# Kernel tuning notes

Hardware: AMD Instinct MI355X
Metric: run time of the kernel (lower is better)

## Reference

```python
import jax, jax.numpy as jnp
import numpy as np

N, E, IN_DIM, H, D = 50000, 1600000, 128, 4, 32
LEAKY_ALPHA = 0.2

def _glorot(key, shape):
    r = np.sqrt(6.0 / (shape[0] + shape[1]))
    return jax.random.uniform(key, shape, jnp.float32, -r, r)

def setup_inputs() -> dict:
    key = jax.random.key(0)
    ks = jax.random.split(key, 6)
    x = jax.random.normal(ks[0], (N, IN_DIM), jnp.float32)
    edge_index = jax.random.randint(ks[1], (2, E), 0, N, jnp.int64 if jax.config.jax_enable_x64 else jnp.int32)
    W_src = _glorot(ks[2], (IN_DIM, H * D))
    W_dst = _glorot(ks[3], (IN_DIM, H * D))
    W_val = _glorot(ks[4], (IN_DIM, H * D))
    attn_vec = _glorot(ks[5], (1, H)).reshape(1, H, 1) * jnp.ones((1, H, D), jnp.float32)
    # faithful glorot for (1,H,D): fan based on shape[0]+shape[1]=1+H as in source
    r = np.sqrt(6.0 / (1 + H))
    attn_vec = jax.random.uniform(jax.random.fold_in(key, 7), (1, H, D), jnp.float32, -r, r)
    return {"x": x, "edge_index": edge_index, "W_src": W_src, "W_dst": W_dst, "W_val": W_val, "attn_vec": attn_vec}

def reference(x, edge_index, W_src, W_dst, W_val, attn_vec):
    n = x.shape[0]
    h = attn_vec.shape[1]
    d = attn_vec.shape[2]
    h_s = (x @ W_src).reshape(n, h, d)
    h_d = (x @ W_dst).reshape(n, h, d)
    h_v = (x @ W_val).reshape(n, h, d)
    src, dst = edge_index[0], edge_index[1]
    # GATv2 edge scores: a^T LeakyReLU(W_src h_i + W_dst h_j)  -> [E, H]
    middle = jax.nn.leaky_relu(h_s[src] + h_d[dst], negative_slope=LEAKY_ALPHA)
    scores = jnp.sum(middle * attn_vec, axis=-1)  # [E, H]
    # segment softmax over incoming edges of each dst node (all heads at once)
    seg_max = jax.ops.segment_max(scores, dst, num_segments=n)  # [N, H]
    exp_scores = jnp.exp(scores - seg_max[dst])
    seg_sum = jax.ops.segment_sum(exp_scores, dst, num_segments=n)
    attn = exp_scores / (seg_sum[dst] + 1e-9)  # [E, H]
    # weighted message aggregation
    messages = (attn[..., None] * h_v[src]).reshape(-1, h * d)  # [E, H*D]
    out_sum = jax.ops.segment_sum(messages, dst, num_segments=n)  # [N, H*D]
    return out_sum, attn
```

## Files before the change

kernel.cpp:

```cpp
#include <hip/hip_runtime.h>

#define LEAKY 0.2f
#define BCAP 512

typedef __attribute__((ext_vector_type(8))) short short8v;
typedef __attribute__((ext_vector_type(4))) float f32x4;

__device__ __forceinline__ float h2f(unsigned short b) {
    union { unsigned short u; _Float16 h; } c; c.u = b; return (float)c.h;
}
__device__ __forceinline__ unsigned short f2h(float f) {
    union { unsigned short u; _Float16 h; } c; c.h = (_Float16)f; return c.u;
}
__device__ __forceinline__ void h4w(unsigned wx, unsigned wy, float& a, float& b, float& c, float& d) {
    a = h2f((unsigned short)(wx & 0xFFFF)); b = h2f((unsigned short)(wx >> 16));
    c = h2f((unsigned short)(wy & 0xFFFF)); d = h2f((unsigned short)(wy >> 16));
}
__device__ __forceinline__ unsigned short f2bf(float f) {
    unsigned u = __float_as_uint(f);
    return (unsigned short)((u + 0x7FFFu + ((u >> 16) & 1u)) >> 16);
}
__device__ __forceinline__ float bf2f(unsigned short b) {
    return __uint_as_float((unsigned)b << 16);
}
__device__ __forceinline__ int clampi(int v, int hi) { return v < 0 ? 0 : (v > hi ? hi : v); }
__device__ __forceinline__ int ld_idx(const int* __restrict__ ei, int is64, size_t pos) {
    return is64 ? ei[pos * 2] : ei[pos];
}

__global__ __launch_bounds__(256) void detect_kernel(const int* __restrict__ ei, int* flag) {
    __shared__ int nz;
    if (threadIdx.x == 0) nz = 0;
    __syncthreads();
    if (ei[2 * threadIdx.x + 1] != 0) atomicOr(&nz, 1);
    __syncthreads();
    if (threadIdx.x == 0) *flag = (nz == 0) ? 1 : 0;
}

__global__ __launch_bounds__(256) void zerob_kernel(int* __restrict__ bcnt, int NB8) {
    int t = blockIdx.x * 256 + threadIdx.x;
    if (t < NB8) bcnt[t] = 0;
}

__global__ __launch_bounds__(256) void bucket_scatter_kernel(
    const int* __restrict__ ei, const int* __restrict__ iflag,
    int* __restrict__ bcnt, uint2* __restrict__ bucket_data, int N, int E)
{
    int t = blockIdx.x * 256 + threadIdx.x;
    if (t >= E) return;
    int is64 = *iflag;
    int src = clampi(ld_idx(ei, is64, (size_t)t), N - 1);
    int dst = clampi(ld_idx(ei, is64, (size_t)E + t), N - 1);
    int slot = (dst >> 6) * 8 + (blockIdx.x & 7);
    int k = atomicAdd(&bcnt[slot], 1);
    if (k < BCAP)
        bucket_data[(size_t)slot * BCAP + k] =
            make_uint2((unsigned)src | ((unsigned)(dst & 63) << 16), (unsigned)t);
}

__global__ __launch_bounds__(256) void bscan_kernel(
    const int* __restrict__ bcnt, int* __restrict__ bbase,
    int* __restrict__ offs, int NB, int N, int E)
{
    __shared__ int buf[256];
    __shared__ int base;
    const int t = threadIdx.x;
    if (t == 0) { base = 0; bbase[0] = 0; offs[N] = E; }
    __syncthreads();
    for (int start = 0; start < NB; start += 256) {
        int i = start + t;
        int v = 0;
        if (i < NB) {
            #pragma unroll
            for (int s = 0; s < 8; ++s) {
                int c = bcnt[i * 8 + s];
                v += (c < BCAP ? c : BCAP);
            }
        }
        buf[t] = v;
        __syncthreads();
        #pragma unroll
        for (int off = 1; off < 256; off <<= 1) {
            int xv = (t >= off) ? buf[t - off] : 0;
            __syncthreads();
            buf[t] += xv;
            __syncthreads();
        }
        if (i < NB) bbase[i + 1] = base + buf[t];
        __syncthreads();
        if (t == 0) base += buf[255];
        __syncthreads();
    }
}

__global__ __launch_bounds__(256) void csr_build_kernel(
    const uint2* __restrict__ bucket_data, const int* __restrict__ bcnt,
    const int* __restrict__ bbase, int* __restrict__ offs,
    int2* __restrict__ sorted2, int N)
{
    __shared__ int cnt[64];
    __shared__ int pre[64];
    __shared__ int scnt[8];
    const int b = blockIdx.x;
    const int t = threadIdx.x;
    if (t < 8) { int c = bcnt[b * 8 + t]; scnt[t] = c < BCAP ? c : BCAP; }
    if (t < 64) cnt[t] = 0;
    __syncthreads();
    const int gbase = bbase[b];
    #pragma unroll
    for (int s = 0; s < 8; ++s) {
        int c = scnt[s];
        const uint2* p = &bucket_data[((size_t)b * 8 + s) * BCAP];
        for (int k = t; k < c; k += 256)
            atomicAdd(&cnt[(p[k].x >> 16) & 63], 1);
    }
    __syncthreads();
    if (t < 64) {
        int v = cnt[t], o = v;
        #pragma unroll
        for (int off = 1; off < 64; off <<= 1) {
            int xv = __shfl_up(v, off);
            if (t >= off) v += xv;
        }
        pre[t] = v - o;
        int node = b * 64 + t;
        if (node < N) offs[node] = gbase + pre[t];
    }
    __syncthreads();
    if (t < 64) cnt[t] = pre[t];
    __syncthreads();
    #pragma unroll
    for (int s = 0; s < 8; ++s) {
        int c = scnt[s];
        const uint2* p = &bucket_data[((size_t)b * 8 + s) * BCAP];
        for (int k = t; k < c; k += 256) {
            uint2 d = p[k];
            int dl = (d.x >> 16) & 63;
            int pos = gbase + atomicAdd(&cnt[dl], 1);
            sorted2[pos] = make_int2((int)(d.x & 0xFFFF), (int)d.y);
        }
    }
}

__global__ __launch_bounds__(256) void wprep_kernel(
    const float* __restrict__ W0, const float* __restrict__ W1, const float* __restrict__ W2,
    uint4* __restrict__ wfrag)
{
    int t = blockIdx.x * 256 + threadIdx.x;
    if (t >= 3 * 8 * 4 * 64) return;
    int lane = t & 63, ks = (t >> 6) & 3, nt = (t >> 8) & 7, w = t >> 11;
    const float* W = (w == 0) ? W0 : ((w == 1) ? W1 : W2);
    int col = nt * 16 + (lane & 15);
    int k0 = ks * 32 + ((lane >> 4) & 3) * 8;
    short8v h, l;
    #pragma unroll
    for (int j = 0; j < 8; ++j) {
        float v = W[(size_t)(k0 + j) * 128 + col];
        unsigned short hb = f2bf(v);
        h[j] = (short)hb;
        l[j] = (short)f2bf(v - bf2f(hb));
    }
    size_t slot = ((size_t)nt * 4 + ks) * 64 + lane;
    *(short8v*)&wfrag[(size_t)w * 4096 + 0 * 2048 + slot] = h;
    *(short8v*)&wfrag[(size_t)w * 4096 + 1 * 2048 + slot] = l;
}

__global__ __launch_bounds__(256) void gemm3_mfma_kernel(
    const float* __restrict__ x, const uint4* __restrict__ wfrag,
    unsigned short* __restrict__ comb_us, float* __restrict__ hd, int N)
{
    __shared__ uint4 wsb4[4096];
    unsigned short* wsb = (unsigned short*)wsb4;
    const int tid = threadIdx.x;
    const int wave = tid >> 6;
    const int lane = tid & 63;
    const int lhi = lane >> 4;
    const int llo = lane & 15;
    const int base_row = blockIdx.x * 128 + wave * 32;

    short8v Ahi[2][4], Alo[2][4];
    #pragma unroll
    for (int rt = 0; rt < 2; ++rt) {
        #pragma unroll
        for (int ks = 0; ks < 4; ++ks) {
            int row = base_row + rt * 16 + llo;
            int rowc = row < N ? row : N - 1;
            const float* p = &x[(size_t)rowc * 128 + ks * 32 + lhi * 8];
            float4 v0 = *(const float4*)p;
            float4 v1 = *(const float4*)(p + 4);
            float vv[8] = {v0.x, v0.y, v0.z, v0.w, v1.x, v1.y, v1.z, v1.w};
            short8v h, l;
            #pragma unroll
            for (int j = 0; j < 8; ++j) {
                unsigned short hb = f2bf(vv[j]);
                h[j] = (short)hb;
                l[j] = (short)f2bf(vv[j] - bf2f(hb));
            }
            Ahi[rt][ks] = h; Alo[rt][ks] = l;
        }
    }

    for (int w = 0; w < 3; ++w) {
        __syncthreads();
        #pragma unroll
        for (int it = 0; it < 16; ++it) {
            int slot = it * 256 + tid;
            wsb4[slot] = wfrag[(size_t)w * 4096 + slot];
        }
        __syncthreads();

        f32x4 acc[2][8];
        #pragma unroll
        for (int rt = 0; rt < 2; ++rt)
            #pragma unroll
            for (int nt = 0; nt < 8; ++nt)
                acc[rt][nt] = (f32x4){0.f, 0.f, 0.f, 0.f};

        #pragma unroll
        for (int ks = 0; ks < 4; ++ks) {
            #pragma unroll
            for (int nt = 0; nt < 8; ++nt) {
                short8v Bh = *(short8v*)&wsb[((((size_t)0 * 8 + nt) * 4 + ks) * 64 + lane) * 8];
                short8v Bl = *(short8v*)&wsb[((((size_t)1 * 8 + nt) * 4 + ks) * 64 + lane) * 8];
                acc[0][nt] = __builtin_amdgcn_mfma_f32_16x16x32_bf16(Ahi[0][ks], Bh, acc[0][nt], 0, 0, 0);
                acc[1][nt] = __builtin_amdgcn_mfma_f32_16x16x32_bf16(Ahi[1][ks], Bh, acc[1][nt], 0, 0, 0);
                acc[0][nt] = __builtin_amdgcn_mfma_f32_16x16x32_bf16(Alo[0][ks], Bh, acc[0][nt], 0, 0, 0);
                acc[1][nt] = __builtin_amdgcn_mfma_f32_16x16x32_bf16(Alo[1][ks], Bh, acc[1][nt], 0, 0, 0);
                acc[0][nt] = __builtin_amdgcn_mfma_f32_16x16x32_bf16(Ahi[0][ks], Bl, acc[0][nt], 0, 0, 0);
                acc[1][nt] = __builtin_amdgcn_mfma_f32_16x16x32_bf16(Ahi[1][ks], Bl, acc[1][nt], 0, 0, 0);
            }
        }

        #pragma unroll
        for (int rt = 0; rt < 2; ++rt) {
            #pragma unroll
            for (int nt = 0; nt < 8; ++nt) {
                #pragma unroll
                for (int reg = 0; reg < 4; ++reg) {
                    int node = base_row + rt * 16 + lhi * 4 + reg;
                    int col = nt * 16 + llo;
                    if (node < N) {
                        float v = acc[rt][nt][reg];
                        if (w == 1) {
                            hd[(size_t)node * 128 + col] = v;
                        } else {
                            int slot = (w == 2) ? 1 : 0;
                            comb_us[(size_t)node * 256 + (col >> 2) * 8 + slot * 4 + (col & 3)] = f2h(v);
                        }
                    }
                }
            }
        }
    }
}

__global__ __launch_bounds__(256) void gather_fused_kernel(
    const int* __restrict__ offs, const int2* __restrict__ sorted2,
    const uint4* __restrict__ comb, const float* __restrict__ hd,
    const float* __restrict__ av,
    float* __restrict__ scores, float* __restrict__ out,
    float* __restrict__ segsum, int N)
{
    int wid = (int)(((size_t)blockIdx.x * 256 + threadIdx.x) >> 6);
    if (wid >= N) return;
    int lane = threadIdx.x & 63;
    int sub = lane >> 5;
    int le = lane & 31;
    int h = le >> 3;
    int beg = offs[wid], end = offs[wid + 1];

    float4 d4 = *(const float4*)&hd[(size_t)wid * 128 + le * 4];
    float4 a4 = *(const float4*)&av[le * 4];

    float sum = 0.f;
    float a0 = 0.f, a1 = 0.f, a2 = 0.f, a3 = 0.f;

    int j = beg + sub;
    int2 se0 = make_int2(0, 0), se1 = make_int2(0, 0);
    uint4 c0 = make_uint4(0, 0, 0, 0);
    if (j < end)     se0 = sorted2[j];
    if (j + 2 < end) se1 = sorted2[j + 2];
    if (j < end)     c0 = comb[(size_t)se0.x * 32 + le];

    while (j < end) {
        int jn = j + 2;
        int2 se2 = make_int2(0, 0);
        uint4 c1 = make_uint4(0, 0, 0, 0);
        if (jn + 2 < end) se2 = sorted2[jn + 2];
        if (jn < end)     c1 = comb[(size_t)se1.x * 32 + le];

        float s0, s1, s2, s3, v0, v1, v2, v3;
        h4w(c0.x, c0.y, s0, s1, s2, s3);
        h4w(c0.z, c0.w, v0, v1, v2, v3);
        float m, s = 0.f;
        m = s0 + d4.x; m = (m > 0.f) ? m : LEAKY * m; s += m * a4.x;
        m = s1 + d4.y; m = (m > 0.f) ? m : LEAKY * m; s += m * a4.y;
        m = s2 + d4.z; m = (m > 0.f) ? m : LEAKY * m; s += m * a4.z;
        m = s3 + d4.w; m = (m > 0.f) ? m : LEAKY * m; s += m * a4.w;
        s += __shfl_xor(s, 1);
        s += __shfl_xor(s, 2);
        s += __shfl_xor(s, 4);
        if ((le & 7) == 0) scores[(size_t)se0.y * 4 + h] = s;
        float w = __expf(s);
        sum += w;
        a0 += w * v0; a1 += w * v1; a2 += w * v2; a3 += w * v3;

        j = jn; se0 = se1; se1 = se2; c0 = c1;
    }
    sum += __shfl_xor(sum, 32);
    a0 += __shfl_xor(a0, 32); a1 += __shfl_xor(a1, 32);
    a2 += __shfl_xor(a2, 32); a3 += __shfl_xor(a3, 32);
    float inv = 1.f / (sum + 1e-9f);
    if (sub == 0) {
        *(float4*)&out[(size_t)wid * 128 + le * 4] =
            make_float4(a0 * inv, a1 * inv, a2 * inv, a3 * inv);
        if ((le & 7) == 0) segsum[(size_t)wid * 4 + h] = sum;
    }
}

__global__ __launch_bounds__(256) void attn_write_kernel(
    const int* __restrict__ ei, const int* __restrict__ iflag,
    float* sc, const float* __restrict__ segsum, int N, int E)
{
    int t = blockIdx.x * 256 + threadIdx.x;
    if (t >= E * 4) return;
    int e = t >> 2, h = t & 3;
    int dst = clampi(ld_idx(ei, *iflag, (size_t)E + e), N - 1);
    sc[t] = __expf(sc[t]) / (segsum[(size_t)dst * 4 + h] + 1e-9f);
}

extern "C" void kernel_launch(void* const* d_in, const int* in_sizes, int n_in,
                              void* d_out, int out_size, void* d_ws, size_t ws_size,
                              hipStream_t stream)
{
    const float* x  = (const float*)d_in[0];
    const int* ei   = (const int*)d_in[1];
    const float* W0 = (const float*)d_in[2];
    const float* W1 = (const float*)d_in[3];
    const float* W2 = (const float*)d_in[4];
    const float* av = (const float*)d_in[5];
    const int N = in_sizes[0] / 128;
    const int E = in_sizes[1] / 2;
    const int NB = (N + 63) >> 6;

    float* out_f = (float*)d_out;
    float* hd = out_f;
    float* out_sum = out_f;
    float* scores = out_f + (size_t)N * 128;

    uint2* bucket_data = (uint2*)d_ws;
    uint4* comb = (uint4*)d_ws;
    size_t ubytes = ((size_t)NB * 8 * BCAP * 8 + 255) & ~(size_t)255;
    int2* sorted2 = (int2*)((char*)d_ws + ubytes);
    float* segsum = (float*)(sorted2 + (size_t)E);
    int* bcnt = (int*)(segsum + (size_t)N * 4);
    int* bbase = bcnt + NB * 8;
    int* offs = bbase + (NB + 1);
    int* iflag = offs + (N + 1);
    uint4* wfrag = (uint4*)(((uintptr_t)(iflag + 1) + 255) & ~(uintptr_t)255);

    detect_kernel<<<1, 256, 0, stream>>>(ei, iflag);
    zerob_kernel<<<(NB * 8 + 255) / 256, 256, 0, stream>>>(bcnt, NB * 8);
    bucket_scatter_kernel<<<(E + 255) / 256, 256, 0, stream>>>(
        ei, iflag, bcnt, bucket_data, N, E);
    bscan_kernel<<<1, 256, 0, stream>>>(bcnt, bbase, offs, NB, N, E);
    csr_build_kernel<<<NB, 256, 0, stream>>>(bucket_data, bcnt, bbase, offs, sorted2, N);
    wprep_kernel<<<24, 256, 0, stream>>>(W0, W1, W2, wfrag);
    gemm3_mfma_kernel<<<(N + 127) / 128, 256, 0, stream>>>(
        x, wfrag, (unsigned short*)comb, hd, N);
    gather_fused_kernel<<<(N + 3) / 4, 256, 0, stream>>>(
        offs, sorted2, comb, hd, av, scores, out_sum, segsum, N);
    attn_write_kernel<<<(E * 4 + 255) / 256, 256, 0, stream>>>(
        ei, iflag, scores, segsum, N, E);
}
```

Before: 383.4 us.

## Merge prep kernels, stage CSR buckets in LDS, use packed fp16 scoring

Merges the detect, zero and weight-prep kernels into one launch to cut launch overhead. The CSR build copies each block's bucket entries into shared memory once instead of reading them from global memory twice. The edge score now uses packed half2 arithmetic with fdot2 and a max/min split for LeakyReLU. The exp'd score is stored directly along with the reciprocal segment sum, so the attention write pass is a single multiply. The fp16 score math lowers precision, and the 32KB LDS buffer may reduce occupancy in csr_build.

After: 379.5 us. Within noise of the previous version (-1.0%).

```diff
diff --git a/kernel.cpp b/kernel.cpp
--- a/kernel.cpp
+++ b/kernel.cpp
@@ -5,12 +5,16 @@
 
 typedef __attribute__((ext_vector_type(8))) short short8v;
 typedef __attribute__((ext_vector_type(4))) float f32x4;
+typedef _Float16 half2v __attribute__((ext_vector_type(2)));
 
 __device__ __forceinline__ float h2f(unsigned short b) {
     union { unsigned short u; _Float16 h; } c; c.u = b; return (float)c.h;
 }
 __device__ __forceinline__ unsigned short f2h(float f) {
     union { unsigned short u; _Float16 h; } c; c.h = (_Float16)f; return c.u;
+}
+__device__ __forceinline__ half2v u2h2(unsigned u) {
+    union { unsigned u; half2v h; } c; c.u = u; return c.h;
 }
 __device__ __forceinline__ void h4w(unsigned wx, unsigned wy, float& a, float& b, float& c, float& d) {
     a = h2f((unsigned short)(wx & 0xFFFF)); b = h2f((unsigned short)(wx >> 16));
@@ -27,19 +31,63 @@
 __device__ __forceinline__ int ld_idx(const int* __restrict__ ei, int is64, size_t pos) {
     return is64 ? ei[pos * 2] : ei[pos];
 }
-
-__global__ __launch_bounds__(256) void detect_kernel(const int* __restrict__ ei, int* flag) {
-    __shared__ int nz;
-    if (threadIdx.x == 0) nz = 0;
-    __syncthreads();
-    if (ei[2 * threadIdx.x + 1] != 0) atomicOr(&nz, 1);
-    __syncthreads();
-    if (threadIdx.x == 0) *flag = (nz == 0) ? 1 : 0;
-}
-
-__global__ __launch_bounds__(256) void zerob_kernel(int* __restrict__ bcnt, int NB8) {
-    int t = blockIdx.x * 256 + threadIdx.x;
-    if (t < NB8) bcnt[t] = 0;
+__device__ __forceinline__ half2v h2max(half2v a, half2v b) {
+#if __has_builtin(__builtin_elementwise_max)
+    return __builtin_elementwise_max(a, b);
+#else
+    half2v r; r.x = a.x > b.x ? a.x : b.x; r.y = a.y > b.y ? a.y : b.y; return r;
+#endif
+}
+__device__ __forceinline__ half2v h2min(half2v a, half2v b) {
+#if __has_builtin(__builtin_elementwise_min)
+    return __builtin_elementwise_min(a, b);
+#else
+    half2v r; r.x = a.x < b.x ? a.x : b.x; r.y = a.y < b.y ? a.y : b.y; return r;
+#endif
+}
+__device__ __forceinline__ float fdot2f(half2v a, half2v b, float c) {
+#if __has_builtin(__builtin_amdgcn_fdot2)
+    return __builtin_amdgcn_fdot2(a, b, c, false);
+#else
+    return (float)a.x * (float)b.x + (float)a.y * (float)b.y + c;
+#endif
+}
+
+__global__ __launch_bounds__(256) void prep_kernel(
+    const int* __restrict__ ei, int* __restrict__ iflag,
+    int* __restrict__ bcnt, int NB8,
+    const float* __restrict__ W0, const float* __restrict__ W1, const float* __restrict__ W2,
+    uint4* __restrict__ wfrag)
+{
+    const int b = blockIdx.x;
+    if (b == 0) {
+        __shared__ int nz;
+        if (threadIdx.x == 0) nz = 0;
+        __syncthreads();
+        if (ei[2 * threadIdx.x + 1] != 0) atomicOr(&nz, 1);
+        __syncthreads();
+        if (threadIdx.x == 0) *iflag = (nz == 0) ? 1 : 0;
+    } else if (b <= 24) {
+        int t = (b - 1) * 256 + threadIdx.x;
+        int lane = t & 63, ks = (t >> 6) & 3, nt = (t >> 8) & 7, w = t >> 11;
+        const float* W = (w == 0) ? W0 : ((w == 1) ? W1 : W2);
+        int col = nt * 16 + (lane & 15);
+        int k0 = ks * 32 + ((lane >> 4) & 3) * 8;
+        short8v h, l;
+        #pragma unroll
+        for (int j = 0; j < 8; ++j) {
+            float v = W[(size_t)(k0 + j) * 128 + col];
+            unsigned short hb = f2bf(v);
+            h[j] = (short)hb;
+            l[j] = (short)f2bf(v - bf2f(hb));
+        }
+        size_t slot = ((size_t)nt * 4 + ks) * 64 + lane;
+        *(short8v*)&wfrag[(size_t)w * 4096 + 0 * 2048 + slot] = h;
+        *(short8v*)&wfrag[(size_t)w * 4096 + 1 * 2048 + slot] = l;
+    } else {
+        int t = (b - 25) * 256 + threadIdx.x;
+        if (t < NB8) bcnt[t] = 0;
+    }
 }
 
 __global__ __launch_bounds__(256) void bucket_scatter_kernel(
@@ -98,23 +146,36 @@
     const int* __restrict__ bbase, int* __restrict__ offs,
     int2* __restrict__ sorted2, int N)
 {
+    __shared__ uint2 ebuf[8 * BCAP];
     __shared__ int cnt[64];
     __shared__ int pre[64];
-    __shared__ int scnt[8];
+    __shared__ int soff[9];
     const int b = blockIdx.x;
     const int t = threadIdx.x;
-    if (t < 8) { int c = bcnt[b * 8 + t]; scnt[t] = c < BCAP ? c : BCAP; }
+    if (t == 0) {
+        int acc = 0;
+        #pragma unroll
+        for (int s = 0; s < 8; ++s) {
+            soff[s] = acc;
+            int c = bcnt[b * 8 + s];
+            acc += (c < BCAP ? c : BCAP);
+        }
+        soff[8] = acc;
+    }
     if (t < 64) cnt[t] = 0;
     __syncthreads();
-    const int gbase = bbase[b];
+    const int tcnt = soff[8];
     #pragma unroll
     for (int s = 0; s < 8; ++s) {
-        int c = scnt[s];
+        int o = soff[s], c = soff[s + 1] - o;
         const uint2* p = &bucket_data[((size_t)b * 8 + s) * BCAP];
-        for (int k = t; k < c; k += 256)
-            atomicAdd(&cnt[(p[k].x >> 16) & 63], 1);
-    }
-    __syncthreads();
+        for (int k = t; k < c; k += 256) ebuf[o + k] = p[k];
+    }
+    __syncthreads();
+    for (int k = t; k < tcnt; k += 256)
+        atomicAdd(&cnt[(ebuf[k].x >> 16) & 63], 1);
+    __syncthreads();
+    const int gbase = bbase[b];
     if (t < 64) {
         int v = cnt[t], o = v;
         #pragma unroll
@@ -129,40 +190,12 @@
     __syncthreads();
     if (t < 64) cnt[t] = pre[t];
     __syncthreads();
-    #pragma unroll
-    for (int s = 0; s < 8; ++s) {
-        int c = scnt[s];
-        const uint2* p = &bucket_data[((size_t)b * 8 + s) * BCAP];
-        for (int k = t; k < c; k += 256) {
-            uint2 d = p[k];
-            int dl = (d.x >> 16) & 63;
-            int pos = gbase + atomicAdd(&cnt[dl], 1);
-            sorted2[pos] = make_int2((int)(d.x & 0xFFFF), (int)d.y);
-        }
-    }
-}
-
-__global__ __launch_bounds__(256) void wprep_kernel(
-    const float* __restrict__ W0, const float* __restrict__ W1, const float* __restrict__ W2,
-    uint4* __restrict__ wfrag)
-{
-    int t = blockIdx.x * 256 + threadIdx.x;
-    if (t >= 3 * 8 * 4 * 64) return;
-    int lane = t & 63, ks = (t >> 6) & 3, nt = (t >> 8) & 7, w = t >> 11;
-    const float* W = (w == 0) ? W0 : ((w == 1) ? W1 : W2);
-    int col = nt * 16 + (lane & 15);
-    int k0 = ks * 32 + ((lane >> 4) & 3) * 8;
-    short8v h, l;
-    #pragma unroll
-    for (int j = 0; j < 8; ++j) {
-        float v = W[(size_t)(k0 + j) * 128 + col];
-        unsigned short hb = f2bf(v);
-        h[j] = (short)hb;
-        l[j] = (short)f2bf(v - bf2f(hb));
-    }
-    size_t slot = ((size_t)nt * 4 + ks) * 64 + lane;
-    *(short8v*)&wfrag[(size_t)w * 4096 + 0 * 2048 + slot] = h;
-    *(short8v*)&wfrag[(size_t)w * 4096 + 1 * 2048 + slot] = l;
+    for (int k = t; k < tcnt; k += 256) {
+        uint2 d = ebuf[k];
+        int dl = (d.x >> 16) & 63;
+        int pos = gbase + atomicAdd(&cnt[dl], 1);
+        sorted2[pos] = make_int2((int)(d.x & 0xFFFF), (int)d.y);
+    }
 }
 
 __global__ __launch_bounds__(256) void gemm3_mfma_kernel(
@@ -271,6 +304,11 @@
 
     float4 d4 = *(const float4*)&hd[(size_t)wid * 128 + le * 4];
     float4 a4 = *(const float4*)&av[le * 4];
+    const half2v d2_0 = {(_Float16)d4.x, (_Float16)d4.y};
+    const half2v d2_1 = {(_Float16)d4.z, (_Float16)d4.w};
+    const half2v av2_0 = {(_Float16)a4.x, (_Float16)a4.y};
+    const half2v av2_1 = {(_Float16)a4.z, (_Float16)a4.w};
+    const half2v hz = {(_Float16)0.f, (_Float16)0.f};
 
     float sum = 0.f;
     float a0 = 0.f, a1 = 0.f, a2 = 0.f, a3 = 0.f;
@@ -289,20 +327,21 @@
         if (jn + 2 < end) se2 = sorted2[jn + 2];
         if (jn < end)     c1 = comb[(size_t)se1.x * 32 + le];
 
-        float s0, s1, s2, s3, v0, v1, v2, v3;
-        h4w(c0.x, c0.y, s0, s1, s2, s3);
-        h4w(c0.z, c0.w, v0, v1, v2, v3);
-        float m, s = 0.f;
-        m = s0 + d4.x; m = (m > 0.f) ? m : LEAKY * m; s += m * a4.x;
-        m = s1 + d4.y; m = (m > 0.f) ? m : LEAKY * m; s += m * a4.y;
-        m = s2 + d4.z; m = (m > 0.f) ? m : LEAKY * m; s += m * a4.z;
-        m = s3 + d4.w; m = (m > 0.f) ? m : LEAKY * m; s += m * a4.w;
+        half2v m0 = u2h2(c0.x) + d2_0;
+        half2v m1 = u2h2(c0.y) + d2_1;
+        half2v p0 = h2max(m0, hz), q0 = h2min(m0, hz);
+        half2v p1 = h2max(m1, hz), q1 = h2min(m1, hz);
+        float sp = fdot2f(p1, av2_1, fdot2f(p0, av2_0, 0.f));
+        float sq = fdot2f(q1, av2_1, fdot2f(q0, av2_0, 0.f));
+        float s = fmaf(LEAKY, sq, sp);
         s += __shfl_xor(s, 1);
         s += __shfl_xor(s, 2);
         s += __shfl_xor(s, 4);
-        if ((le & 7) == 0) scores[(size_t)se0.y * 4 + h] = s;
         float w = __expf(s);
+        if ((le & 7) == 0) scores[(size_t)se0.y * 4 + h] = w;
         sum += w;
+        float v0, v1, v2, v3;
+        h4w(c0.z, c0.w, v0, v1, v2, v3);
         a0 += w * v0; a1 += w * v1; a2 += w * v2; a3 += w * v3;
 
         j = jn; se0 = se1; se1 = se2; c0 = c1;
@@ -314,7 +353,7 @@
     if (sub == 0) {
         *(float4*)&out[(size_t)wid * 128 + le * 4] =
             make_float4(a0 * inv, a1 * inv, a2 * inv, a3 * inv);
-        if ((le & 7) == 0) segsum[(size_t)wid * 4 + h] = sum;
+        if ((le & 7) == 0) segsum[(size_t)wid * 4 + h] = inv;
     }
 }
 
@@ -326,7 +365,7 @@
     if (t >= E * 4) return;
     int e = t >> 2, h = t & 3;
     int dst = clampi(ld_idx(ei, *iflag, (size_t)E + e), N - 1);
-    sc[t] = __expf(sc[t]) / (segsum[(size_t)dst * 4 + h] + 1e-9f);
+    sc[t] = sc[t] * segsum[(size_t)dst * 4 + h];
 }
 
 extern "C" void kernel_launch(void* const* d_in, const int* in_sizes, int n_in,
@@ -359,13 +398,12 @@
     int* iflag = offs + (N + 1);
     uint4* wfrag = (uint4*)(((uintptr_t)(iflag + 1) + 255) & ~(uintptr_t)255);
 
-    detect_kernel<<<1, 256, 0, stream>>>(ei, iflag);
-    zerob_kernel<<<(NB * 8 + 255) / 256, 256, 0, stream>>>(bcnt, NB * 8);
+    const int zblocks = (NB * 8 + 255) / 256;
+    prep_kernel<<<25 + zblocks, 256, 0, stream>>>(ei, iflag, bcnt, NB * 8, W0, W1, W2, wfrag);
     bucket_scatter_kernel<<<(E + 255) / 256, 256, 0, stream>>>(
         ei, iflag, bcnt, bucket_data, N, E);
     bscan_kernel<<<1, 256, 0, stream>>>(bcnt, bbase, offs, NB, N, E);
     csr_build_kernel<<<NB, 256, 0, stream>>>(bucket_data, bcnt, bbase, offs, sorted2, N);
-    wprep_kernel<<<24, 256, 0, stream>>>(W0, W1, W2, wfrag);
     gemm3_mfma_kernel<<<(N + 127) / 128, 256, 0, stream>>>(
         x, wfrag, (unsigned short*)comb, hd, N);
     gather_fused_kernel<<<(N + 3) / 4, 256, 0, stream>>>(
```
